# Kernel optimization log

Hardware: AMD Instinct MI355X
Metric: run time of the kernel (lower is better)

The kernel has to match this reference:

```python
import jax, jax.numpy as jnp
import numpy as np

B, S, D, NH = 2, 1024, 2048, 8
QK, V, I = 1024, 2048, 8192  # qk_dim = D/2, v_dim = D, intermediate = 4D
CAP = 15.0
EPS = 1e-6


def setup_inputs() -> dict:
    key = jax.random.key(0)
    ks = jax.random.split(key, 12)
    sc = D ** -0.5
    return {
        "x": jax.random.normal(ks[0], (B, S, D), jnp.float32),
        "Wq": jax.random.normal(ks[1], (D, QK), jnp.float32) * sc,
        "Wk": jax.random.normal(ks[2], (D, QK), jnp.float32) * sc,
        "Wv": jax.random.normal(ks[3], (D, V), jnp.float32) * sc,
        "Wo": jax.random.normal(ks[4], (D, V), jnp.float32) * sc,
        "Wi": jax.random.normal(ks[5], (D, NH), jnp.float32) * sc,
        "bi": -10.0 * jnp.ones((NH,), jnp.float32),   # xLSTM input-gate bias init
        "Wf": jax.random.normal(ks[6], (D, NH), jnp.float32) * sc,
        "bf": jnp.linspace(3.0, 6.0, NH, dtype=jnp.float32),  # forget-gate bias init
        "mh_norm_w": jnp.ones((V,), jnp.float32),
        "Wout": jax.random.normal(ks[7], (V, D), jnp.float32) * (V ** -0.5),
        "rms1_w": jnp.ones((D,), jnp.float32),
        "Wgate": jax.random.normal(ks[8], (D, I), jnp.float32) * sc,
        "Wup": jax.random.normal(ks[9], (D, I), jnp.float32) * sc,
        "Wdown": jax.random.normal(ks[10], (I, D), jnp.float32) * (I ** -0.5),
        "rms2_w": jnp.ones((D,), jnp.float32),
    }


def soft_cap(x, cap=CAP):
    return cap * jnp.tanh(x / cap)


def rms_norm(x, w, eps=EPS):
    xf = x.astype(jnp.float32)
    var = jnp.mean(xf * xf, axis=-1, keepdims=True)
    return (w * (xf * jax.lax.rsqrt(var + eps))).astype(x.dtype)


def mlstm_stabilized(q, k, v, i, f):
    # q,k: [B,NH,S,DQK]; v: [B,NH,S,DV]; i,f: [B,NH,S] (soft-capped preacts)
    dqk = q.shape[-1]
    logf = jax.nn.log_sigmoid(f.astype(jnp.float32))
    lfc = jnp.cumsum(logf, axis=-1)                         # [B,NH,S]
    tri = jnp.tril(jnp.ones((S, S), bool))
    # log decay D[t,s] = sum_{j=s+1..t} log sig(f_j) + i_s  (causal)
    logD = jnp.where(tri, lfc[..., :, None] - lfc[..., None, :], -jnp.inf) + i[..., None, :]
    m = jnp.max(logD, axis=-1, keepdims=True)               # [B,NH,S,1] stabilizer
    Dm = jnp.exp(logD - m)
    scores = jnp.einsum("bhsd,bhtd->bhst", q, k) * (dqk ** -0.5) * Dm
    n = jnp.maximum(jnp.abs(scores.sum(-1, keepdims=True)), jnp.exp(-m))
    return jnp.einsum("bhst,bhtv->bhsv", scores, v) / (n + EPS)  # [B,NH,S,DV]


def xlstm_layer(x, Wq, Wk, Wv, Wo, Wi, bi, Wf, bf, mh_norm_w, Wout):
    q = (x @ Wq).reshape(B, S, NH, -1).transpose(0, 2, 1, 3)
    k = (x @ Wk).reshape(B, S, NH, -1).transpose(0, 2, 1, 3)
    v = (x @ Wv).reshape(B, S, NH, -1).transpose(0, 2, 1, 3)
    o_preact = x @ Wo                                       # [B,S,V]
    i = soft_cap(x @ Wi + bi).transpose(0, 2, 1)            # [B,NH,S]
    f = soft_cap(x @ Wf + bf).transpose(0, 2, 1)
    h = mlstm_stabilized(q, k, v, i, f)                     # [B,NH,S,DV]
    h = h.transpose(0, 2, 1, 3)                             # [B,S,NH,DV]
    # multi-head RMS norm over per-head value dim
    hf = h.astype(jnp.float32)
    var = jnp.mean(hf * hf, axis=-1, keepdims=True)
    hn = (hf * jax.lax.rsqrt(var + EPS)).reshape(B, S, V) * mh_norm_w
    h_out = jax.nn.sigmoid(o_preact) * hn                   # output gate
    return h_out @ Wout


def reference(x, Wq, Wk, Wv, Wo, Wi, bi, Wf, bf, mh_norm_w, Wout, rms1_w,
              Wgate, Wup, Wdown, rms2_w):
    residual = x
    h = xlstm_layer(x, Wq, Wk, Wv, Wo, Wi, bi, Wf, bf, mh_norm_w, Wout)
    h = residual + rms_norm(h, rms1_w)
    mlp = (jax.nn.silu(h @ Wgate) * (h @ Wup)) @ Wdown
    return h + rms_norm(mlp, rms2_w)
```

## Files before the change

kernel.cpp:

```cpp
#include <hip/hip_runtime.h>
#include <hip/hip_bf16.h>

#define TOKENS 2048
#define DMODEL 2048
#define SEQ    1024
#define QKVO   6144

typedef __attribute__((ext_vector_type(8))) short bf16x8;
typedef __attribute__((ext_vector_type(4))) short bf16x4;
typedef __attribute__((ext_vector_type(4))) float f32x4;
typedef __attribute__((ext_vector_type(8))) unsigned short u16x8;
typedef __attribute__((ext_vector_type(4))) unsigned short u16x4;

__device__ __forceinline__ float sigmoidf_(float x) { return 1.f / (1.f + expf(-x)); }
__device__ __forceinline__ float softcapf_(float x) { return 15.f * tanhf(x * (1.f / 15.f)); }
__device__ __forceinline__ float logsigf_(float x) {
  return (x >= 0.f) ? -log1pf(expf(-x)) : (x - log1pf(expf(x)));
}
__device__ __forceinline__ unsigned short f2bf(float f) {
  unsigned u = __builtin_bit_cast(unsigned, f);
  u += 0x7FFFu + ((u >> 16) & 1u);
  return (unsigned short)(u >> 16);
}
__device__ __forceinline__ float bf2f(unsigned short b) {
  unsigned u = ((unsigned)b) << 16;
  return __builtin_bit_cast(float, u);
}

typedef __attribute__((address_space(3))) void lds_void;
typedef const __attribute__((address_space(1))) void gmem_void;
__device__ __forceinline__ void gload16(const void* g, void* l) {
  __builtin_amdgcn_global_load_lds((gmem_void*)g, (lds_void*)l, 16, 0, 0);
}
__device__ __forceinline__ unsigned lds_off(const void* p) {
  return (unsigned)(size_t)(__attribute__((address_space(3))) const void*)p;
}

#if defined(__has_builtin)
#if __has_builtin(__builtin_amdgcn_mfma_f32_16x16x16bf16_1k)
#define HAVE_MFMA16 1
#endif
#endif

__device__ __forceinline__ f32x4 mfma16_bf16(bf16x4 a, bf16x4 b, f32x4 c) {
#ifdef HAVE_MFMA16
  return __builtin_amdgcn_mfma_f32_16x16x16bf16_1k(a, b, c, 0, 0, 0);
#else
  f32x4 d;
  asm volatile("v_mfma_f32_16x16x16_bf16 %0, %1, %2, %3"
               : "=v"(d) : "v"(a), "v"(b), "v"(c));
  return d;
#endif
}

__device__ __forceinline__ bf16x4 tr_read(unsigned addr) {
  bf16x4 d;
  asm volatile("ds_read_b64_tr_b16 %0, %1" : "=v"(d) : "v"(addr));
  return d;
}

__device__ __forceinline__ void remap_block(int& bm, int& bn) {
  const int nbx = gridDim.x, nby = gridDim.y;
  const int bid = blockIdx.y * nbx + blockIdx.x;
  const int q = (nbx * nby) >> 3;
  const int lid = (bid & 7) * q + (bid >> 3);
  bm = lid % nby;
  bn = lid / nby;
}

template <int EPI>
__global__ __launch_bounds__(512) void gemm256(
    const unsigned short* __restrict__ A, const unsigned short* __restrict__ BT,
    void* __restrict__ Cout, const unsigned short* __restrict__ aux,
    int M, int N, int K, int ldk) {
  __shared__ unsigned short lds[3][2][8192];
  const int tid = threadIdx.x;
  int bm, bn;
  remap_block(bm, bn);
  const int m0 = bm * 256, n0 = bn * 256;
  const int wid = tid >> 6, lane = tid & 63;
  const int wr = wid >> 2, wc = wid & 3;
  const int fr = lane & 15, fq = lane >> 4;
  const size_t kz = (size_t)blockIdx.z * K;

  const f32x4 zero = {0.f, 0.f, 0.f, 0.f};
  f32x4 acc[8][4];
#pragma unroll
  for (int m = 0; m < 8; ++m)
#pragma unroll
    for (int n = 0; n < 4; ++n) acc[m][n] = zero;

  const int sr = tid >> 2;
  const int sc = tid & 3;
  const int sgc = sc ^ ((sr + (sr >> 2)) & 3);
  const unsigned short* Asrc = A + kz + (size_t)(m0 + sr) * ldk + sgc * 8;
  const unsigned short* Bsrc = BT + kz + (size_t)(n0 + sr) * ldk + sgc * 8;
  const size_t hstep = (size_t)128 * ldk;
  const int ldst = sr * 32 + sc * 8;

  const int rsw = (fq ^ ((fr + (fr >> 2)) & 3)) * 8;
  const int arow0 = wr * 128 + fr;
  const int brow0 = wc * 64 + fr;

  auto stage = [&](int t) {
    const size_t ko = (size_t)t * 32;
    const int bs = t % 3;
    gload16(Asrc + ko, &lds[bs][0][ldst]);
    gload16(Asrc + ko + hstep, &lds[bs][0][4096 + ldst]);
    gload16(Bsrc + ko, &lds[bs][1][ldst]);
    gload16(Bsrc + ko + hstep, &lds[bs][1][4096 + ldst]);
  };

  const int NT = K >> 5;
  stage(0);
  stage(1);

  for (int t = 0; t < NT; ++t) {
    if (t + 1 < NT) {
      asm volatile("s_waitcnt vmcnt(4)" ::: "memory");
    } else {
      asm volatile("s_waitcnt vmcnt(0)" ::: "memory");
    }
    __builtin_amdgcn_s_barrier();
    if (t + 2 < NT) stage(t + 2);
    const int b = t % 3;
    const unsigned short* la = &lds[b][0][0];
    const unsigned short* lb = &lds[b][1][0];
    bf16x8 bfm[4], af[4];
#pragma unroll
    for (int n = 0; n < 4; ++n)
      bfm[n] = *(const bf16x8*)&lb[(brow0 + n * 16) * 32 + rsw];
#pragma unroll
    for (int m = 0; m < 4; ++m)
      af[m] = *(const bf16x8*)&la[(arow0 + m * 16) * 32 + rsw];
    __builtin_amdgcn_s_setprio(1);
#pragma unroll
    for (int m = 0; m < 4; ++m)
#pragma unroll
      for (int n = 0; n < 4; ++n)
        acc[m][n] = __builtin_amdgcn_mfma_f32_16x16x32_bf16(af[m], bfm[n],
                                                            acc[m][n], 0, 0, 0);
    __builtin_amdgcn_s_setprio(0);
#pragma unroll
    for (int m = 0; m < 4; ++m)
      af[m] = *(const bf16x8*)&la[(arow0 + 64 + m * 16) * 32 + rsw];
    __builtin_amdgcn_s_setprio(1);
#pragma unroll
    for (int m = 0; m < 4; ++m)
#pragma unroll
      for (int n = 0; n < 4; ++n)
        acc[4 + m][n] = __builtin_amdgcn_mfma_f32_16x16x32_bf16(
            af[m], bfm[n], acc[4 + m][n], 0, 0, 0);
    __builtin_amdgcn_s_setprio(0);
  }

  const int orow = m0 + wr * 128 + fq * 4;
  const int ocol = n0 + wc * 64 + fr;
#pragma unroll
  for (int m = 0; m < 8; ++m) {
#pragma unroll
    for (int n = 0; n < 4; ++n) {
      const int cc = ocol + n * 16;
#pragma unroll
      for (int j = 0; j < 4; ++j) {
        const int r = orow + m * 16 + j;
        float v = acc[m][n][j];
        if (EPI == 0) {
          ((float*)Cout + (size_t)blockIdx.z * M * N)[(size_t)r * N + cc] = v;
        } else if (EPI == 1) {
          ((unsigned short*)Cout)[(size_t)r * N + cc] = f2bf(v);
        } else {
          const size_t idx = (size_t)r * N + cc;
          const float gv = bf2f(aux[idx]);
          ((unsigned short*)Cout)[idx] = f2bf(v * gv * sigmoidf_(gv));
        }
      }
    }
  }
}

template <int EPI>
__global__ __launch_bounds__(256) void gemm_bf16(
    const unsigned short* __restrict__ A, const unsigned short* __restrict__ BT,
    void* __restrict__ Cout, int M, int N, int K) {
  __shared__ unsigned short As[2][128 * 32];
  __shared__ unsigned short Bs[2][128 * 32];
  const int tid = threadIdx.x;
  int bm, bn;
  remap_block(bm, bn);
  const int m0 = bm * 128;
  const int n0 = bn * 128;
  const int wid = tid >> 6;
  const int lane = tid & 63;
  const int wr = wid >> 1, wc = wid & 1;
  const int fr = lane & 15, fq = lane >> 4;

  const f32x4 zero = {0.f, 0.f, 0.f, 0.f};
  f32x4 acc[4][4];
#pragma unroll
  for (int m = 0; m < 4; ++m)
#pragma unroll
    for (int n = 0; n < 4; ++n) acc[m][n] = zero;

  const int srow = tid >> 2;
  const int sc = tid & 3;
  const int sgc = sc ^ ((srow + (srow >> 2)) & 3);
  const int scol = sgc * 8;
  const unsigned short* Ag0 = A + (size_t)(m0 + srow) * K + scol;
  const unsigned short* Ag1 = A + (size_t)(m0 + 64 + srow) * K + scol;
  const unsigned short* Bg0 = BT + (size_t)(n0 + srow) * K + scol;
  const unsigned short* Bg1 = BT + (size_t)(n0 + 64 + srow) * K + scol;
  const int rsw = (fq ^ ((fr + (fr >> 2)) & 3)) * 8;

  gload16(Ag0, &As[0][tid * 8]);
  gload16(Ag1, &As[0][2048 + tid * 8]);
  gload16(Bg0, &Bs[0][tid * 8]);
  gload16(Bg1, &Bs[0][2048 + tid * 8]);
  __syncthreads();

  const int nt = K >> 5;
  for (int t = 0; t < nt; ++t) {
    const int cur = t & 1;
    if (t + 1 < nt) {
      const int k0 = (t + 1) << 5;
      gload16(Ag0 + k0, &As[cur ^ 1][tid * 8]);
      gload16(Ag1 + k0, &As[cur ^ 1][2048 + tid * 8]);
      gload16(Bg0 + k0, &Bs[cur ^ 1][tid * 8]);
      gload16(Bg1 + k0, &Bs[cur ^ 1][2048 + tid * 8]);
    }
    bf16x8 af[4], bfm[4];
#pragma unroll
    for (int m = 0; m < 4; ++m)
      af[m] = *(const bf16x8*)&As[cur][(wr * 64 + m * 16 + fr) * 32 + rsw];
#pragma unroll
    for (int n = 0; n < 4; ++n)
      bfm[n] = *(const bf16x8*)&Bs[cur][(wc * 64 + n * 16 + fr) * 32 + rsw];
    __builtin_amdgcn_s_setprio(1);
#pragma unroll
    for (int m = 0; m < 4; ++m)
#pragma unroll
      for (int n = 0; n < 4; ++n)
        acc[m][n] = __builtin_amdgcn_mfma_f32_16x16x32_bf16(af[m], bfm[n],
                                                            acc[m][n], 0, 0, 0);
    __builtin_amdgcn_s_setprio(0);
    __syncthreads();
  }

  const int orow = m0 + wr * 64 + fq * 4;
  const int ocol = n0 + wc * 64 + fr;
#pragma unroll
  for (int m = 0; m < 4; ++m) {
#pragma unroll
    for (int n = 0; n < 4; ++n) {
      const int cc = ocol + n * 16;
#pragma unroll
      for (int j = 0; j < 4; ++j) {
        const int r = orow + m * 16 + j;
        float v = acc[m][n][j];
        if (EPI == 0) ((float*)Cout)[(size_t)r * N + cc] = v;
        else ((unsigned short*)Cout)[(size_t)r * N + cc] = f2bf(v);
      }
    }
  }
}

__global__ __launch_bounds__(256) void castT_kernel(
    const float* __restrict__ W, unsigned short* __restrict__ WT, int K, int N) {
  __shared__ float tile[128][65];
  const int n0 = blockIdx.x * 64, k0 = blockIdx.y * 128;
  const int rr = threadIdx.x >> 4;
  const int c4 = (threadIdx.x & 15) * 4;
#pragma unroll
  for (int p = 0; p < 8; ++p) {
    const int r = p * 16 + rr;
    float4 v = *(const float4*)&W[(size_t)(k0 + r) * N + n0 + c4];
    tile[r][c4 + 0] = v.x; tile[r][c4 + 1] = v.y;
    tile[r][c4 + 2] = v.z; tile[r][c4 + 3] = v.w;
  }
  __syncthreads();
  const int kc = (threadIdx.x & 15) * 8;
#pragma unroll
  for (int p = 0; p < 4; ++p) {
    const int n = p * 16 + rr;
    u16x8 o;
#pragma unroll
    for (int j = 0; j < 8; ++j) o[j] = f2bf(tile[kc + j][n]);
    *(u16x8*)&WT[(size_t)(n0 + n) * K + k0 + kc] = o;
  }
}

__global__ __launch_bounds__(256) void gatesT_kernel(
    const float* __restrict__ Wi, const float* __restrict__ Wf,
    float* __restrict__ WT) {
  const int idx = blockIdx.x * 256 + threadIdx.x;
  const int row = idx >> 11;
  const int d = idx & 2047;
  const float* W = (row < 8) ? Wi : Wf;
  WT[idx] = W[d * 8 + (row & 7)];
}

__global__ __launch_bounds__(256) void gates_kernel(
    const float* __restrict__ x, const float* __restrict__ WT,
    const float* __restrict__ bi, const float* __restrict__ bf,
    float* __restrict__ icap, float* __restrict__ fls,
    unsigned short* __restrict__ xb) {
  const int t = blockIdx.x;
  const int tid = threadIdx.x;
  __shared__ float xs[2048];
  *(float4*)&xs[tid * 4] = *(const float4*)&x[(size_t)t * 2048 + tid * 4];
  *(float4*)&xs[1024 + tid * 4] =
      *(const float4*)&x[(size_t)t * 2048 + 1024 + tid * 4];
  __syncthreads();
  {
    u16x8 o;
#pragma unroll
    for (int j = 0; j < 8; ++j) o[j] = f2bf(xs[tid * 8 + j]);
    *(u16x8*)&xb[(size_t)t * 2048 + tid * 8] = o;
  }
  const int wave = tid >> 6, lane = tid & 63;
  const int b = t >> 10, s = t & 1023;
  for (int gg = wave; gg < 16; gg += 4) {
    const int head = gg & 7;
    const int isF = gg >> 3;
    const float* Wrow = WT + (size_t)gg * 2048;
    float acc = 0.f;
#pragma unroll
    for (int it = 0; it < 8; ++it) {
      const float4 w4 = *(const float4*)&Wrow[it * 256 + lane * 4];
      const float4 x4 = *(const float4*)&xs[it * 256 + lane * 4];
      acc = fmaf(x4.x, w4.x, acc);
      acc = fmaf(x4.y, w4.y, acc);
      acc = fmaf(x4.z, w4.z, acc);
      acc = fmaf(x4.w, w4.w, acc);
    }
#pragma unroll
    for (int m = 32; m > 0; m >>= 1) acc += __shfl_down(acc, m, 64);
    if (lane == 0) {
      const size_t o = (size_t)(b * 8 + head) * 1024 + s;
      if (isF) fls[o] = logsigf_(softcapf_(acc + bf[head]));
      else icap[o] = softcapf_(acc + bi[head]);
    }
  }
}

__global__ __launch_bounds__(1024) void scan_kernel(
    const float* __restrict__ icap, const float* __restrict__ fls,
    float* __restrict__ lfc, float* __restrict__ garr, float* __restrict__ mx) {
  const int bh = blockIdx.x;
  const int tid = threadIdx.x;
  __shared__ float sm[1024];
  sm[tid] = fls[(size_t)bh * 1024 + tid];
  __syncthreads();
  for (int off = 1; off < 1024; off <<= 1) {
    float v = sm[tid];
    if (tid >= off) v += sm[tid - off];
    __syncthreads();
    sm[tid] = v;
    __syncthreads();
  }
  const float l = sm[tid];
  lfc[(size_t)bh * 1024 + tid] = l;
  const float g = icap[(size_t)bh * 1024 + tid] - l;
  garr[(size_t)bh * 1024 + tid] = g;
  __syncthreads();
  sm[tid] = g;
  __syncthreads();
  for (int off = 1; off < 1024; off <<= 1) {
    float v = sm[tid];
    if (tid >= off) v = fmaxf(v, sm[tid - off]);
    __syncthreads();
    sm[tid] = v;
    __syncthreads();
  }
  mx[(size_t)bh * 1024 + tid] = sm[tid];
}

__global__ __launch_bounds__(256) void mlstm_mfma_kernel(
    const unsigned short* __restrict__ qkvob,
    const float* __restrict__ garr, const float* __restrict__ lfc,
    const float* __restrict__ mx, float* __restrict__ h) {
  __shared__ unsigned short k_lds[32 * 128];
  __shared__ unsigned short v_lds[32 * 256];
  const int tid = threadIdx.x;
  const int lane = tid & 63;
  const int w = tid >> 6;
  const int bh = blockIdx.y;
  const int b = bh >> 3, hh = bh & 7;
  const int tb = blockIdx.x;
  const int fr = lane & 15, fq = lane >> 4;
  const int tw = tb * 64 + w * 16 + fr;
  const size_t tokT = (size_t)(b * SEQ + tw);
  const float scale = 0.08838834764831845f;

  bf16x8 qf[4];
#pragma unroll
  for (int kd = 0; kd < 4; ++kd)
    qf[kd] = *(const bf16x8*)&qkvob[tokT * QKVO + hh * 128 + kd * 32 + fq * 8];

  const float Mt = mx[(size_t)bh * SEQ + tw];
  const float mt = lfc[(size_t)bh * SEQ + tw] + Mt;

  f32x4 acc[16];
  const f32x4 zero = {0.f, 0.f, 0.f, 0.f};
#pragma unroll
  for (int D = 0; D < 16; ++D) acc[D] = zero;
  float asum = 0.f;

  const unsigned vbase = lds_off(v_lds);
  const int nsb = tb * 2 + 2;

  for (int sb = 0; sb < nsb; ++sb) {
    const int s0 = sb * 32;
    if (sb) __syncthreads();
#pragma unroll
    for (int it = 0; it < 2; ++it) {
      const int ck = it * 256 + tid;
      const int s = ck >> 4, c = ck & 15;
      const int cg = c ^ (s & 7);
      gload16(&qkvob[(size_t)(b * SEQ + s0 + s) * QKVO + 1024 + hh * 128 + cg * 8],
              &k_lds[ck * 8]);
    }
#pragma unroll
    for (int it = 0; it < 4; ++it) {
      const int cv = it * 256 + tid;
      const int W_ = cv >> 9, D = (cv >> 5) & 15, g = (cv >> 3) & 3,
                jj = (cv >> 1) & 3, c2 = cv & 1;
      const int s = W_ * 16 + g * 4 + jj;
      gload16(&qkvob[(size_t)(b * SEQ + s0 + s) * QKVO + 2048 + hh * 256 +
                     D * 16 + c2 * 8],
              &v_lds[cv * 8]);
    }
    __syncthreads();

#pragma unroll
    for (int st = 0; st < 2; ++st) {
      f32x4 cfrag = zero;
      const int srow = st * 16 + fr;
#pragma unroll
      for (int kd = 0; kd < 4; ++kd) {
        const int cc = (kd * 4 + fq) ^ (srow & 7);
        const bf16x8 kf = *(const bf16x8*)&k_lds[srow * 128 + cc * 8];
        cfrag = __builtin_amdgcn_mfma_f32_16x16x32_bf16(kf, qf[kd], cfrag, 0, 0, 0);
      }
      const int sbase = s0 + st * 16 + fq * 4;
      const float4 g4 = *(const float4*)&garr[(size_t)bh * SEQ + sbase];
      float wv[4];
      wv[0] = (sbase + 0 <= tw) ? cfrag[0] * scale * __expf(g4.x - Mt) : 0.f;
      wv[1] = (sbase + 1 <= tw) ? cfrag[1] * scale * __expf(g4.y - Mt) : 0.f;
      wv[2] = (sbase + 2 <= tw) ? cfrag[2] * scale * __expf(g4.z - Mt) : 0.f;
      wv[3] = (sbase + 3 <= tw) ? cfrag[3] * scale * __expf(g4.w - Mt) : 0.f;
      asum += wv[0] + wv[1] + wv[2] + wv[3];
      bf16x4 pf;
      pf[0] = (short)f2bf(wv[0]); pf[1] = (short)f2bf(wv[1]);
      pf[2] = (short)f2bf(wv[2]); pf[3] = (short)f2bf(wv[3]);

#pragma unroll
      for (int Dg = 0; Dg < 2; ++Dg) {
        bf16x4 vf[8];
#pragma unroll
        for (int D = 0; D < 8; ++D)
          vf[D] = tr_read(vbase + (st * 4096 + (Dg * 8 + D) * 256) * 2 + lane * 8);
        asm volatile("s_waitcnt lgkmcnt(0)" ::: "memory");
        __builtin_amdgcn_sched_barrier(0);
#pragma unroll
        for (int D = 0; D < 8; ++D)
          acc[Dg * 8 + D] = mfma16_bf16(vf[D], pf, acc[Dg * 8 + D]);
      }
    }
  }

  asum += __shfl_xor(asum, 16, 64);
  asum += __shfl_xor(asum, 32, 64);
  const float n = fmaxf(fabsf(asum), __expf(-mt));
  const float inv = 1.f / (n + 1e-6f);
  asm volatile("s_nop 7\n\ts_nop 7" ::);
  float* hrow = &h[tokT * 2048 + hh * 256];
#pragma unroll
  for (int D = 0; D < 16; ++D) {
    float4 o4;
    o4.x = acc[D][0] * inv;
    o4.y = acc[D][1] * inv;
    o4.z = acc[D][2] * inv;
    o4.w = acc[D][3] * inv;
    *(float4*)&hrow[D * 16 + fq * 4] = o4;
  }
}

__global__ __launch_bounds__(256) void hout_kernel(
    const float* __restrict__ h, const unsigned short* __restrict__ qkvob,
    const float* __restrict__ mhw, unsigned short* __restrict__ houtb) {
  const int t = blockIdx.x;
  const int tid = threadIdx.x;
  const size_t base = (size_t)t * 2048 + tid * 8;
  float vals[8];
  *(float4*)&vals[0] = *(const float4*)&h[base];
  *(float4*)&vals[4] = *(const float4*)&h[base + 4];
  float ss = 0.f;
#pragma unroll
  for (int j = 0; j < 8; ++j) ss += vals[j] * vals[j];
#pragma unroll
  for (int m = 16; m > 0; m >>= 1) ss += __shfl_xor(ss, m, 32);
  const float rinv = rsqrtf(ss * (1.f / 256.f) + 1e-6f);
  const u16x8 ovb = *(const u16x8*)&qkvob[(size_t)t * QKVO + 4096 + tid * 8];
  u16x8 res;
#pragma unroll
  for (int j = 0; j < 8; ++j) {
    const float hn = vals[j] * rinv * mhw[tid * 8 + j];
    res[j] = f2bf(hn * sigmoidf_(bf2f(ovb[j])));
  }
  *(u16x8*)&houtb[base] = res;
}

template <int EMIT_BF16, int NY>
__global__ __launch_bounds__(256) void addrms_kernel(
    const float* __restrict__ base_, const float* __restrict__ y0,
    const float* __restrict__ y1, const float* __restrict__ y2,
    const float* __restrict__ y3, const float* __restrict__ w,
    float* __restrict__ outp, unsigned short* __restrict__ outb) {
  const int t = blockIdx.x;
  const int tid = threadIdx.x;
  __shared__ float red[4];
  const size_t boff = (size_t)t * 2048 + tid * 8;
  float vals[8];
  *(float4*)&vals[0] = *(const float4*)&y0[boff];
  *(float4*)&vals[4] = *(const float4*)&y0[boff + 4];
  if (NY == 4) {
    float v1[8];
    *(float4*)&v1[0] = *(const float4*)&y1[boff];
    *(float4*)&v1[4] = *(const float4*)&y1[boff + 4];
#pragma unroll
    for (int j = 0; j < 8; ++j) vals[j] += v1[j];
    *(float4*)&v1[0] = *(const float4*)&y2[boff];
    *(float4*)&v1[4] = *(const float4*)&y2[boff + 4];
#pragma unroll
    for (int j = 0; j < 8; ++j) vals[j] += v1[j];
    *(float4*)&v1[0] = *(const float4*)&y3[boff];
    *(float4*)&v1[4] = *(const float4*)&y3[boff + 4];
#pragma unroll
    for (int j = 0; j < 8; ++j) vals[j] += v1[j];
  }
  float ss = 0.f;
#pragma unroll
  for (int j = 0; j < 8; ++j) ss += vals[j] * vals[j];
#pragma unroll
  for (int m = 32; m > 0; m >>= 1) ss += __shfl_xor(ss, m, 64);
  if ((tid & 63) == 0) red[tid >> 6] = ss;
  __syncthreads();
  ss = red[0] + red[1] + red[2] + red[3];
  const float rinv = rsqrtf(ss * (1.f / 2048.f) + 1e-6f);
  float bv[8];
  *(float4*)&bv[0] = *(const float4*)&base_[boff];
  *(float4*)&bv[4] = *(const float4*)&base_[boff + 4];
  float res[8];
  u16x8 rb;
#pragma unroll
  for (int j = 0; j < 8; ++j) {
    res[j] = bv[j] + vals[j] * rinv * w[tid * 8 + j];
    if (EMIT_BF16) rb[j] = f2bf(res[j]);
  }
  *(float4*)&outp[boff] = *(float4*)&res[0];
  *(float4*)&outp[boff + 4] = *(float4*)&res[4];
  if (EMIT_BF16) *(u16x8*)&outb[boff] = rb;
}

extern "C" void kernel_launch(void* const* d_in, const int* in_sizes, int n_in,
                              void* d_out, int out_size, void* d_ws,
                              size_t ws_size, hipStream_t stream) {
  const float* x = (const float*)d_in[0];
  const float* Wq = (const float*)d_in[1];
  const float* Wk = (const float*)d_in[2];
  const float* Wv = (const float*)d_in[3];
  const float* Wo = (const float*)d_in[4];
  const float* Wi = (const float*)d_in[5];
  const float* bi = (const float*)d_in[6];
  const float* Wf = (const float*)d_in[7];
  const float* bf = (const float*)d_in[8];
  const float* mhw = (const float*)d_in[9];
  const float* Wout = (const float*)d_in[10];
  const float* rms1 = (const float*)d_in[11];
  const float* Wgate = (const float*)d_in[12];
  const float* Wup = (const float*)d_in[13];
  const float* Wdown = (const float*)d_in[14];
  const float* rms2 = (const float*)d_in[15];
  float* out = (float*)d_out;
  char* base = (char*)d_ws;
  const size_t MBy = 1024 * 1024;

  unsigned short* W = (unsigned short*)(base);
  unsigned short* actb = (unsigned short*)(base + 32 * MBy);
  float* gs = (float*)(base + 48 * MBy);
  unsigned short* houtb = (unsigned short*)(base + 48 * MBy);
  float* h = (float*)(base + 64 * MBy);
  float* f1 = (float*)(base + 64 * MBy);
  unsigned short* gbuf = (unsigned short*)(base + 80 * MBy);
  float* mlp = (float*)(base + 80 * MBy);
  unsigned short* xb = (unsigned short*)(base + 112 * MBy);
  unsigned short* f1b = (unsigned short*)(base + 112 * MBy);
  unsigned short* qkvob = (unsigned short*)(base + 120 * MBy);
  float* attn = (float*)(base + 120 * MBy);
  float* icap = gs;
  float* fls = gs + 16384;
  float* lfc = gs + 32768;
  float* garr = gs + 49152;
  float* mxp = gs + 65536;
  float* gwT = gs + 81920;

  const dim3 blk(256);

  gatesT_kernel<<<128, blk, 0, stream>>>(Wi, Wf, gwT);
  gates_kernel<<<TOKENS, blk, 0, stream>>>(x, gwT, bi, bf, icap, fls, xb);
  scan_kernel<<<16, 1024, 0, stream>>>(icap, fls, lfc, garr, mxp);

  castT_kernel<<<dim3(16, 16), blk, 0, stream>>>(Wq, W, 2048, 1024);
  castT_kernel<<<dim3(16, 16), blk, 0, stream>>>(Wk, W + (size_t)1024 * 2048,
                                                 2048, 1024);
  castT_kernel<<<dim3(32, 16), blk, 0, stream>>>(Wv, W + (size_t)2048 * 2048,
                                                 2048, 2048);
  castT_kernel<<<dim3(32, 16), blk, 0, stream>>>(Wo, W + (size_t)4096 * 2048,
                                                 2048, 2048);
  gemm256<1><<<dim3(24, 8), dim3(512), 0, stream>>>(
      xb, W, qkvob, nullptr, TOKENS, 6144, 2048, 2048);

  mlstm_mfma_kernel<<<dim3(16, 16), dim3(256), 0, stream>>>(qkvob, garr, lfc,
                                                            mxp, h);
  hout_kernel<<<TOKENS, blk, 0, stream>>>(h, qkvob, mhw, houtb);

  castT_kernel<<<dim3(32, 16), blk, 0, stream>>>(Wout, W, 2048, 2048);
  gemm_bf16<0><<<dim3(16, 16), blk, 0, stream>>>(houtb, W, attn, TOKENS, 2048,
                                                 2048);

  addrms_kernel<1, 1><<<TOKENS, blk, 0, stream>>>(
      x, attn, nullptr, nullptr, nullptr, rms1, f1, f1b);

  castT_kernel<<<dim3(128, 16), blk, 0, stream>>>(Wgate, W, 2048, 8192);
  gemm256<1><<<dim3(32, 8), dim3(512), 0, stream>>>(
      f1b, W, gbuf, nullptr, TOKENS, 8192, 2048, 2048);
  castT_kernel<<<dim3(128, 16), blk, 0, stream>>>(Wup, W, 2048, 8192);
  gemm256<2><<<dim3(32, 8), dim3(512), 0, stream>>>(
      f1b, W, actb, gbuf, TOKENS, 8192, 2048, 2048);

  castT_kernel<<<dim3(32, 64), blk, 0, stream>>>(Wdown, W, 8192, 2048);
  gemm256<0><<<dim3(8, 8, 4), dim3(512), 0, stream>>>(
      actb, W, mlp, nullptr, TOKENS, 2048, 2048, 8192);

  addrms_kernel<0, 4><<<TOKENS, blk, 0, stream>>>(
      f1, mlp, mlp + 4194304, mlp + 8388608, mlp + 12582912, rms2, out,
      nullptr);
}
```

Before: 517.8 us.

## Fuse gate/up GEMMs into dual GEMM and fold head norm into mLSTM

Replaces the separate gate GEMM (bf16 intermediate written and re-read) and up GEMM with one dual-B GEMM. Each block loads the A tile once and computes both gate and up accumulators, then applies SiLU(g)*u in the epilogue. Also moves the multi-head RMS norm and output-gate sigmoid into the mLSTM kernel epilogue, removing the fp32 h buffer and the hout kernel launch. In exchange the dual GEMM uses a narrower 128-column N tile with twice the accumulators, and the mLSTM kernel carries more registers.

```diff
diff --git a/kernel.cpp b/kernel.cpp
--- a/kernel.cpp
+++ b/kernel.cpp
@@ -71,8 +71,7 @@
 template <int EPI>
 __global__ __launch_bounds__(512) void gemm256(
     const unsigned short* __restrict__ A, const unsigned short* __restrict__ BT,
-    void* __restrict__ Cout, const unsigned short* __restrict__ aux,
-    int M, int N, int K, int ldk) {
+    void* __restrict__ Cout, int M, int N, int K, int ldk) {
   __shared__ unsigned short lds[3][2][8192];
   const int tid = threadIdx.x;
   int bm, bn;
@@ -167,13 +166,119 @@
         float v = acc[m][n][j];
         if (EPI == 0) {
           ((float*)Cout + (size_t)blockIdx.z * M * N)[(size_t)r * N + cc] = v;
-        } else if (EPI == 1) {
+        } else {
           ((unsigned short*)Cout)[(size_t)r * N + cc] = f2bf(v);
-        } else {
-          const size_t idx = (size_t)r * N + cc;
-          const float gv = bf2f(aux[idx]);
-          ((unsigned short*)Cout)[idx] = f2bf(v * gv * sigmoidf_(gv));
         }
+      }
+    }
+  }
+}
+
+__global__ __launch_bounds__(512) void gemm_dual(
+    const unsigned short* __restrict__ A, const unsigned short* __restrict__ BT1,
+    const unsigned short* __restrict__ BT2, unsigned short* __restrict__ Cout,
+    int M, int N, int K) {
+  __shared__ unsigned short lds[3][16384];
+  const int tid = threadIdx.x;
+  int bm, bn;
+  remap_block(bm, bn);
+  const int m0 = bm * 256, n0 = bn * 128;
+  const int wid = tid >> 6, lane = tid & 63;
+  const int wr = wid >> 2, wc = wid & 3;
+  const int fr = lane & 15, fq = lane >> 4;
+
+  const f32x4 zero = {0.f, 0.f, 0.f, 0.f};
+  f32x4 acc1[8][2], acc2[8][2];
+#pragma unroll
+  for (int m = 0; m < 8; ++m)
+#pragma unroll
+    for (int n = 0; n < 2; ++n) { acc1[m][n] = zero; acc2[m][n] = zero; }
+
+  const int sr = tid >> 2;
+  const int sc = tid & 3;
+  const int sgc = sc ^ ((sr + (sr >> 2)) & 3);
+  const unsigned short* Asrc = A + (size_t)(m0 + sr) * K + sgc * 8;
+  const unsigned short* B1src = BT1 + (size_t)(n0 + sr) * K + sgc * 8;
+  const unsigned short* B2src = BT2 + (size_t)(n0 + sr) * K + sgc * 8;
+  const size_t hstep = (size_t)128 * K;
+  const int ldst = sr * 32 + sc * 8;
+
+  const int rsw = (fq ^ ((fr + (fr >> 2)) & 3)) * 8;
+  const int arow0 = wr * 128 + fr;
+  const int brow0 = wc * 32 + fr;
+
+  auto stage = [&](int t) {
+    const size_t ko = (size_t)t * 32;
+    const int bs = t % 3;
+    gload16(Asrc + ko, &lds[bs][ldst]);
+    gload16(Asrc + ko + hstep, &lds[bs][4096 + ldst]);
+    gload16(B1src + ko, &lds[bs][8192 + ldst]);
+    gload16(B2src + ko, &lds[bs][12288 + ldst]);
+  };
+
+  const int NT = K >> 5;
+  stage(0);
+  stage(1);
+
+  for (int t = 0; t < NT; ++t) {
+    if (t + 1 < NT) {
+      asm volatile("s_waitcnt vmcnt(4)" ::: "memory");
+    } else {
+      asm volatile("s_waitcnt vmcnt(0)" ::: "memory");
+    }
+    __builtin_amdgcn_s_barrier();
+    if (t + 2 < NT) stage(t + 2);
+    const int b = t % 3;
+    const unsigned short* la = &lds[b][0];
+    bf16x8 b1[2], b2[2], af[4];
+#pragma unroll
+    for (int n = 0; n < 2; ++n) {
+      b1[n] = *(const bf16x8*)&la[8192 + (brow0 + n * 16) * 32 + rsw];
+      b2[n] = *(const bf16x8*)&la[12288 + (brow0 + n * 16) * 32 + rsw];
+    }
+#pragma unroll
+    for (int m = 0; m < 4; ++m)
+      af[m] = *(const bf16x8*)&la[(arow0 + m * 16) * 32 + rsw];
+    __builtin_amdgcn_s_setprio(1);
+#pragma unroll
+    for (int m = 0; m < 4; ++m)
+#pragma unroll
+      for (int n = 0; n < 2; ++n) {
+        acc1[m][n] = __builtin_amdgcn_mfma_f32_16x16x32_bf16(af[m], b1[n],
+                                                             acc1[m][n], 0, 0, 0);
+        acc2[m][n] = __builtin_amdgcn_mfma_f32_16x16x32_bf16(af[m], b2[n],
+                                                             acc2[m][n], 0, 0, 0);
+      }
+    __builtin_amdgcn_s_setprio(0);
+#pragma unroll
+    for (int m = 0; m < 4; ++m)
+      af[m] = *(const bf16x8*)&la[(arow0 + 64 + m * 16) * 32 + rsw];
+    __builtin_amdgcn_s_setprio(1);
+#pragma unroll
+    for (int m = 0; m < 4; ++m)
+#pragma unroll
+      for (int n = 0; n < 2; ++n) {
+        acc1[4 + m][n] = __builtin_amdgcn_mfma_f32_16x16x32_bf16(
+            af[m], b1[n], acc1[4 + m][n], 0, 0, 0);
+        acc2[4 + m][n] = __builtin_amdgcn_mfma_f32_16x16x32_bf16(
+            af[m], b2[n], acc2[4 + m][n], 0, 0, 0);
+      }
+    __builtin_amdgcn_s_setprio(0);
+  }
+
+  const int orow = m0 + wr * 128 + fq * 4;
+  const int ocol = n0 + wc * 32 + fr;
+#pragma unroll
+  for (int m = 0; m < 8; ++m) {
+#pragma unroll
+    for (int n = 0; n < 2; ++n) {
+      const int cc = ocol + n * 16;
+#pragma unroll
+      for (int j = 0; j < 4; ++j) {
+        const int r = orow + m * 16 + j;
+        const float g = acc1[m][n][j];
+        const float u = acc2[m][n][j];
+        Cout[(size_t)r * N + cc] = f2bf(g * sigmoidf_(g) * u);
       }
     }
   }
@@ -378,7 +483,8 @@
 __global__ __launch_bounds__(256) void mlstm_mfma_kernel(
     const unsigned short* __restrict__ qkvob,
     const float* __restrict__ garr, const float* __restrict__ lfc,
-    const float* __restrict__ mx, float* __restrict__ h) {
+    const float* __restrict__ mx, const float* __restrict__ mhw,
+    unsigned short* __restrict__ houtb) {
   __shared__ unsigned short k_lds[32 * 128];
   __shared__ unsigned short v_lds[32 * 256];
   const int tid = threadIdx.x;
@@ -471,44 +577,38 @@
 
   asum += __shfl_xor(asum, 16, 64);
   asum += __shfl_xor(asum, 32, 64);
-  const float n = fmaxf(fabsf(asum), __expf(-mt));
-  const float inv = 1.f / (n + 1e-6f);
+  const float nrm = fmaxf(fabsf(asum), __expf(-mt));
+  const float inv = 1.f / (nrm + 1e-6f);
   asm volatile("s_nop 7\n\ts_nop 7" ::);
-  float* hrow = &h[tokT * 2048 + hh * 256];
+
+  float hv[16][4];
+  float ss = 0.f;
+#pragma unroll
+  for (int D = 0; D < 16; ++D)
+#pragma unroll
+    for (int j = 0; j < 4; ++j) {
+      const float v = acc[D][j] * inv;
+      hv[D][j] = v;
+      ss += v * v;
+    }
+  ss += __shfl_xor(ss, 16, 64);
+  ss += __shfl_xor(ss, 32, 64);
+  const float rinv = rsqrtf(ss * (1.f / 256.f) + 1e-6f);
+  unsigned short* hrow = &houtb[tokT * 2048 + hh * 256];
+  const unsigned short* orow = &qkvob[tokT * QKVO + 4096 + hh * 256];
+  const float* mrow = &mhw[hh * 256];
 #pragma unroll
   for (int D = 0; D < 16; ++D) {
-    float4 o4;
-    o4.x = acc[D][0] * inv;
-    o4.y = acc[D][1] * inv;
-    o4.z = acc[D][2] * inv;
-    o4.w = acc[D][3] * inv;
-    *(float4*)&hrow[D * 16 + fq * 4] = o4;
-  }
-}
-
-__global__ __launch_bounds__(256) void hout_kernel(
-    const float* __restrict__ h, const unsigned short* __restrict__ qkvob,
-    const float* __restrict__ mhw, unsigned short* __restrict__ houtb) {
-  const int t = blockIdx.x;
-  const int tid = threadIdx.x;
-  const size_t base = (size_t)t * 2048 + tid * 8;
-  float vals[8];
-  *(float4*)&vals[0] = *(const float4*)&h[base];
-  *(float4*)&vals[4] = *(const float4*)&h[base + 4];
-  float ss = 0.f;
-#pragma unroll
-  for (int j = 0; j < 8; ++j) ss += vals[j] * vals[j];
-#pragma unroll
-  for (int m = 16; m > 0; m >>= 1) ss += __shfl_xor(ss, m, 32);
-  const float rinv = rsqrtf(ss * (1.f / 256.f) + 1e-6f);
-  const u16x8 ovb = *(const u16x8*)&qkvob[(size_t)t * QKVO + 4096 + tid * 8];
-  u16x8 res;
-#pragma unroll
-  for (int j = 0; j < 8; ++j) {
-    const float hn = vals[j] * rinv * mhw[tid * 8 + j];
-    res[j] = f2bf(hn * sigmoidf_(bf2f(ovb[j])));
-  }
-  *(u16x8*)&houtb[base] = res;
+    const int d0 = D * 16 + fq * 4;
+    const float4 m4 = *(const float4*)&mrow[d0];
+    const u16x4 o4 = *(const u16x4*)&orow[d0];
+    u16x4 res;
+    res[0] = f2bf(hv[D][0] * rinv * m4.x * sigmoidf_(bf2f(o4[0])));
+    res[1] = f2bf(hv[D][1] * rinv * m4.y * sigmoidf_(bf2f(o4[1])));
+    res[2] = f2bf(hv[D][2] * rinv * m4.z * sigmoidf_(bf2f(o4[2])));
+    res[3] = f2bf(hv[D][3] * rinv * m4.w * sigmoidf_(bf2f(o4[3])));
+    *(u16x4*)&hrow[d0] = res;
+  }
 }
 
 template <int EMIT_BF16, int NY>
@@ -589,10 +689,9 @@
   unsigned short* W = (unsigned short*)(base);
   unsigned short* actb = (unsigned short*)(base + 32 * MBy);
   float* gs = (float*)(base + 48 * MBy);
-  unsigned short* houtb = (unsigned short*)(base + 48 * MBy);
-  float* h = (float*)(base + 64 * MBy);
+  unsigned short* houtb = (unsigned short*)(base + 56 * MBy);
   float* f1 = (float*)(base + 64 * MBy);
-  unsigned short* gbuf = (unsigned short*)(base + 80 * MBy);
+  unsigned short* WupT = (unsigned short*)(base + 80 * MBy);
   float* mlp = (float*)(base + 80 * MBy);
   unsigned short* xb = (unsigned short*)(base + 112 * MBy);
   unsigned short* f1b = (unsigned short*)(base + 112 * MBy);
@@ -619,11 +718,10 @@
   castT_kernel<<<dim3(32, 16), blk, 0, stream>>>(Wo, W + (size_t)4096 * 2048,
                                                  2048, 2048);
   gemm256<1><<<dim3(24, 8), dim3(512), 0, stream>>>(
-      xb, W, qkvob, nullptr, TOKENS, 6144, 2048, 2048);
-
-  mlstm_mfma_kernel<<<dim3(16, 16), dim3(256), 0, stream>>>(qkvob, garr, lfc,
-                                                            mxp, h);
-  hout_kernel<<<TOKENS, blk, 0, stream>>>(h, qkvob, mhw, houtb);
+      xb, W, qkvob, TOKENS, 6144, 2048, 2048);
+
+  mlstm_mfma_kernel<<<dim3(16, 16), dim3(256), 0, stream>>>(
+      qkvob, garr, lfc, mxp, mhw, houtb);
 
   castT_kernel<<<dim3(32, 16), blk, 0, stream>>>(Wout, W, 2048, 2048);
   gemm_bf16<0><<<dim3(16, 16), blk, 0, stream>>>(houtb, W, attn, TOKENS, 2048,
@@ -633,15 +731,13 @@
       x, attn, nullptr, nullptr, nullptr, rms1, f1, f1b);
 
   castT_kernel<<<dim3(128, 16), blk, 0, stream>>>(Wgate, W, 2048, 8192);
-  gemm256<1><<<dim3(32, 8), dim3(512), 0, stream>>>(
-      f1b, W, gbuf, nullptr, TOKENS, 8192, 2048, 2048);
-  castT_kernel<<<dim3(128, 16), blk, 0, stream>>>(Wup, W, 2048, 8192);
-  gemm256<2><<<dim3(32, 8), dim3(512), 0, stream>>>(
-      f1b, W, actb, gbuf, TOKENS, 8192, 2048, 2048);
+  castT_kernel<<<dim3(128, 16), blk, 0, stream>>>(Wup, WupT, 2048, 8192);
+  gemm_dual<<<dim3(64, 8), dim3(512), 0, stream>>>(f1b, W, WupT, actb,
+                                                   TOKENS, 8192, 2048);
 
   castT_kernel<<<dim3(32, 64), blk, 0, stream>>>(Wdown, W, 8192, 2048);
   gemm256<0><<<dim3(8, 8, 4), dim3(512), 0, stream>>>(
-      actb, W, mlp, nullptr, TOKENS, 2048, 2048, 8192);
+      actb, W, mlp, TOKENS, 2048, 2048, 8192);
 
   addrms_kernel<0, 4><<<TOKENS, blk, 0, stream>>>(
       f1, mlp, mlp + 4194304, mlp + 8388608, mlp + 12582912, rms2, out,
```

Result: faster. 505.0 us (-2.5%).
